# Kernel optimization log

Hardware: AMD Instinct MI355X
Metric: run time of the kernel (lower is better)

Reference implementation:

```python
import jax, jax.numpy as jnp
import numpy as np

NUM_CLASSES = 100
CLUSTERS_PER_CLASS = 64
LATENT_DIM = 128
BATCH = 32768


def setup_inputs() -> dict:
    key = jax.random.key(0)
    kx, kc, kl = jax.random.split(key, 3)
    x = jax.random.normal(kx, (BATCH, LATENT_DIM), dtype=jnp.float32)
    # nn.Parameter(torch.randn(C, Kc, D) * 0.1)
    centers = jax.random.normal(kc, (NUM_CLASSES, CLUSTERS_PER_CLASS, LATENT_DIM), dtype=jnp.float32) * 0.1
    labels = jax.random.randint(kl, (BATCH,), 0, NUM_CLASSES, dtype=jnp.int64)
    return {"x": x, "centers": centers, "labels": labels}


def reference(x, centers, labels):
    # [C, Kc, D] -> [K, D]
    all_centers = centers.reshape(-1, LATENT_DIM).astype(x.dtype)
    x2 = jnp.sum(x * x, axis=-1, keepdims=True)            # [B,1]
    c2 = jnp.sum(all_centers * all_centers, axis=-1)       # [K]
    sq = x2 + c2[None, :] - 2.0 * jnp.einsum('bd,kd->bk', x, all_centers)
    distances = jnp.sqrt(jnp.maximum(sq, 0.0))             # [B,K]
    closest_indices = jnp.argmin(distances, axis=1)        # [B]
    class_predictions = closest_indices // CLUSTERS_PER_CLASS
    cluster_assignments = closest_indices % CLUSTERS_PER_CLASS
    quantized_hard = all_centers[closest_indices]          # [B,D]
    min_distances = jnp.take_along_axis(distances, closest_indices[:, None], axis=1)[:, 0]
    # straight-through estimator (training path in the torch module)
    quantized = x + jax.lax.stop_gradient(quantized_hard - x)
    return quantized, cluster_assignments, min_distances, class_predictions
```

## Files before the change

kernel.cpp:

```cpp
#include <hip/hip_runtime.h>
#include <math.h>

#define BATCH  32768
#define D      128
#define K      6400
#define KC     64
#define ROWS_PER_BLOCK 128
#define CHUNK_C 128
#define HALVES 2
#define CHUNKS_PER_HALF 25

typedef _Float16 half8 __attribute__((ext_vector_type(8)));
typedef float    floatx4 __attribute__((ext_vector_type(4)));

typedef __attribute__((address_space(3))) unsigned       lds_uint;
typedef __attribute__((address_space(1))) const unsigned glb_uint;

__device__ __forceinline__ void async_lds16(const void* g, void* l) {
    __builtin_amdgcn_global_load_lds((glb_uint*)g, (lds_uint*)l, 16, 0, 0);
}

__global__ __launch_bounds__(256) void pack_kernel(const float* __restrict__ centers,
                                                   _Float16* __restrict__ wh,
                                                   float* __restrict__ c2n) {
    int tid = blockIdx.x * 256 + threadIdx.x;
    int ch = tid >> 11;
    int u  = (tid >> 7) & 15;
    int cw = tid & 127;
    int center = ch * CHUNK_C + cw;
    const float* src = centers + (size_t)center * D + u * 8;
    float4 a = *(const float4*)src;
    float4 b = *(const float4*)(src + 4);
    float f[8] = {a.x, a.y, a.z, a.w, b.x, b.y, b.z, b.w};
    half8 h;
#pragma unroll
    for (int j = 0; j < 8; ++j) h[j] = (_Float16)f[j];
    *(half8*)(wh + (size_t)tid * 8) = h;

    if (blockIdx.x < K / KC) {
        int c_local = threadIdx.x >> 2, part = threadIdx.x & 3;
        int c = blockIdx.x * 64 + c_local;
        const float4* p = (const float4*)(centers + (size_t)c * D + part * 32);
        float s = 0.f;
#pragma unroll
        for (int i = 0; i < 8; ++i) {
            float4 v = p[i];
            s = fmaf(v.x, v.x, s); s = fmaf(v.y, v.y, s);
            s = fmaf(v.z, v.z, s); s = fmaf(v.w, v.w, s);
        }
        s += __shfl_xor(s, 1, 64);
        s += __shfl_xor(s, 2, 64);
        if (part == 0) c2n[c] = -0.5f * s;
    }
}

__global__ __launch_bounds__(512, 4) void dist_kernel(
    const float* __restrict__ x, const float* __restrict__ centers,
    const _Float16* __restrict__ wh, const float* __restrict__ c2n,
    float* __restrict__ ws_sq, int* __restrict__ ws_ix) {
    __shared__ char lds[65536];

    const int t    = threadIdx.x;
    const int w    = t >> 6;
    const int L    = t & 63;
    const int quad = L >> 4;
    const int n16  = L & 15;
    const int rq      = w >> 1;
    const int chalf   = w & 1;
    const int half = blockIdx.y;
    const int gr0  = blockIdx.x * ROWS_PER_BLOCK;

    half8 Ah[2][4];
#pragma unroll
    for (int rt = 0; rt < 2; ++rt) {
        int r = gr0 + rq * 32 + rt * 16 + n16;
        const float* xr = x + (size_t)r * D + quad * 8;
#pragma unroll
        for (int ks = 0; ks < 4; ++ks) {
            float4 a = *(const float4*)(xr + ks * 32);
            float4 b = *(const float4*)(xr + ks * 32 + 4);
            float f[8] = {a.x, a.y, a.z, a.w, b.x, b.y, b.z, b.w};
            half8 h;
#pragma unroll
            for (int j = 0; j < 8; ++j) h[j] = (_Float16)f[j];
            Ah[rt][ks] = h;
        }
    }

    float b1[8], b2[8];
    int   j1_[8], j2_[8];
#pragma unroll
    for (int k = 0; k < 8; ++k) { b1[k] = -3.4e38f; b2[k] = -3.4e38f; j1_[k] = 0; j2_[k] = 0; }

    const char* gh = (const char*)wh + (size_t)half * CHUNKS_PER_HALF * 32768;

#pragma unroll
    for (int i = 0; i < 4; ++i) {
        int seg = w + i * 8;
        async_lds16(gh + seg * 1024 + L * 16, lds + seg * 1024);
    }
    __syncthreads();

    for (int ci = 0; ci < CHUNKS_PER_HALF; ++ci) {
        const char* cur = lds + (ci & 1) * 32768;
        if (ci + 1 < CHUNKS_PER_HALF) {
            const char* gn = gh + (ci + 1) * 32768;
            char* nxt = lds + ((ci + 1) & 1) * 32768;
#pragma unroll
            for (int i = 0; i < 4; ++i) {
                int seg = w + i * 8;
                async_lds16(gn + seg * 1024 + L * 16, nxt + seg * 1024);
            }
        }

        const int kbase = (half * CHUNKS_PER_HALF + ci) * CHUNK_C + chalf * 64;
        float c2v[4];
#pragma unroll
        for (int ct = 0; ct < 4; ++ct) c2v[ct] = c2n[kbase + ct * 16 + n16];

        floatx4 acc[2][4];
#pragma unroll
        for (int rt = 0; rt < 2; ++rt)
#pragma unroll
            for (int ct = 0; ct < 4; ++ct)
                acc[rt][ct] = (floatx4){c2v[ct], c2v[ct], c2v[ct], c2v[ct]};

#pragma unroll
        for (int ks = 0; ks < 4; ++ks) {
            const half8* pb = (const half8*)cur + (ks * 4 + quad) * 128 + chalf * 64 + n16;
#pragma unroll
            for (int ct = 0; ct < 4; ++ct) {
                half8 Bf = pb[ct * 16];
                acc[0][ct] = __builtin_amdgcn_mfma_f32_16x16x32_f16(Ah[0][ks], Bf, acc[0][ct], 0, 0, 0);
                acc[1][ct] = __builtin_amdgcn_mfma_f32_16x16x32_f16(Ah[1][ks], Bf, acc[1][ct], 0, 0, 0);
            }
        }

        int i0 = kbase + n16;
#pragma unroll
        for (int rt = 0; rt < 2; ++rt)
#pragma unroll
            for (int reg = 0; reg < 4; ++reg) {
                float s0 = acc[rt][0][reg], s1 = acc[rt][1][reg];
                float s2 = acc[rt][2][reg], s3 = acc[rt][3][reg];
                bool g01 = s1 > s0, g23 = s3 > s2;
                float m01 = g01 ? s1 : s0;  int x01 = g01 ? i0 + 16 : i0;
                float m23 = g23 ? s3 : s2;  int x23 = g23 ? i0 + 48 : i0 + 32;
                bool gq = m23 > m01;
                float v  = gq ? m23 : m01;  int vi = gq ? x23 : x01;
                int k = rt * 4 + reg;
                bool bet1 = v > b1[k];
                bool bet2 = v > b2[k];
                float nb2 = bet1 ? b1[k] : (bet2 ? v : b2[k]);
                int   nj2 = bet1 ? j1_[k] : (bet2 ? vi : j2_[k]);
                b1[k]  = bet1 ? v : b1[k];
                j1_[k] = bet1 ? vi : j1_[k];
                b2[k]  = nb2;
                j2_[k] = nj2;
            }

        __syncthreads();
    }

    int* candL = (int*)lds;

#pragma unroll
    for (int k = 0; k < 8; ++k) {
        float v1 = b1[k], v2 = b2[k];
        int   p1 = j1_[k], p2 = j2_[k];
#pragma unroll
        for (int m = 1; m < 8; m <<= 1) {
            float o1 = __shfl_xor(v1, m, 64), o2 = __shfl_xor(v2, m, 64);
            int   q1 = __shfl_xor(p1, m, 64), q2 = __shfl_xor(p2, m, 64);
            bool firstMine = (v1 > o1) || (v1 == o1 && p1 < q1);
            float nv1 = firstMine ? v1 : o1;  int np1 = firstMine ? p1 : q1;
            float cb  = firstMine ? o1 : v1;  int cpi = firstMine ? q1 : p1;
            float ob  = firstMine ? v2 : o2;  int obi = firstMine ? p2 : q2;
            bool secOwn = (ob > cb) || (ob == cb && obi < cpi);
            v1 = nv1; p1 = np1;
            v2 = secOwn ? ob : cb;  p2 = secOwn ? obi : cpi;
        }
        if ((n16 & 7) == 0) {
            int rloc = rq * 32 + (k >> 2) * 16 + quad * 4 + (k & 3);
            int g = chalf * 2 + (n16 >> 3);
            candL[rloc * 8 + g * 2 + 0] = p1;
            candL[rloc * 8 + g * 2 + 1] = p2;
        }
    }
    __syncthreads();

    {
        int r = t >> 2, p = t & 3;
        int ixa = candL[r * 8 + p * 2 + 0];
        int ixb = candL[r * 8 + p * 2 + 1];
        const float4* xr4 = (const float4*)(x + (size_t)(gr0 + r) * D);
        const float4* ca4 = (const float4*)(centers + (size_t)ixa * D);
        const float4* cb4 = (const float4*)(centers + (size_t)ixb * D);
        float dota = 0.f, dotb = 0.f, x2s = 0.f, c2a = 0.f, c2b = 0.f;
#pragma unroll
        for (int d4 = 0; d4 < 32; ++d4) {
            float4 xv = xr4[d4], av = ca4[d4], bv = cb4[d4];
            dota = fmaf(xv.x, av.x, dota); dota = fmaf(xv.y, av.y, dota);
            dota = fmaf(xv.z, av.z, dota); dota = fmaf(xv.w, av.w, dota);
            dotb = fmaf(xv.x, bv.x, dotb); dotb = fmaf(xv.y, bv.y, dotb);
            dotb = fmaf(xv.z, bv.z, dotb); dotb = fmaf(xv.w, bv.w, dotb);
            x2s = fmaf(xv.x, xv.x, x2s); x2s = fmaf(xv.y, xv.y, x2s);
            x2s = fmaf(xv.z, xv.z, x2s); x2s = fmaf(xv.w, xv.w, x2s);
            c2a = fmaf(av.x, av.x, c2a); c2a = fmaf(av.y, av.y, c2a);
            c2a = fmaf(av.z, av.z, c2a); c2a = fmaf(av.w, av.w, c2a);
            c2b = fmaf(bv.x, bv.x, c2b); c2b = fmaf(bv.y, bv.y, c2b);
            c2b = fmaf(bv.z, bv.z, c2b); c2b = fmaf(bv.w, bv.w, c2b);
        }
        float sqa = x2s + c2a - 2.f * dota;
        float sqb = x2s + c2b - 2.f * dotb;
        bool aw = (sqa < sqb) || (sqa == sqb && ixa < ixb);
        float sq = aw ? sqa : sqb;
        int   ix = aw ? ixa : ixb;
#pragma unroll
        for (int m = 1; m < 4; m <<= 1) {
            float osq = __shfl_xor(sq, m, 64);
            int   oix = __shfl_xor(ix, m, 64);
            if (osq < sq || (osq == sq && oix < ix)) { sq = osq; ix = oix; }
        }
        if (p == 0) {
            ws_sq[(size_t)half * BATCH + gr0 + r] = sq;
            ws_ix[(size_t)half * BATCH + gr0 + r] = ix;
        }
    }
}

__global__ __launch_bounds__(256) void final_kernel(
    const float* __restrict__ x, const float* __restrict__ centers,
    const float* __restrict__ ws_sq, const int* __restrict__ ws_ix,
    float* __restrict__ out) {
    int g = blockIdx.x * 256 + threadIdx.x;
    int row = g >> 5, d4 = g & 31;

    float sqa = ws_sq[row],         sqb = ws_sq[BATCH + row];
    int   ixa = ws_ix[row],         ixb = ws_ix[BATCH + row];
    bool aw = (sqa <= sqb);
    float sq = aw ? sqa : sqb;
    int   ix = aw ? ixa : ixb;

    float* out_clu = out + (size_t)BATCH * D;
    float* out_md  = out_clu + BATCH;
    float* out_cls = out_md + BATCH;
    if (d4 == 0) {
        out_md[row]  = sqrtf(fmaxf(sq, 0.f));
        out_clu[row] = (float)(ix & (KC - 1));
        out_cls[row] = (float)(ix >> 6);
    }

    float4 cv = ((const float4*)centers)[(size_t)ix * 32 + d4];
    float4 xv = ((const float4*)x)[(size_t)row * 32 + d4];
    float4 o;
    o.x = xv.x + (cv.x - xv.x);
    o.y = xv.y + (cv.y - xv.y);
    o.z = xv.z + (cv.z - xv.z);
    o.w = xv.w + (cv.w - xv.w);
    ((float4*)out)[(size_t)row * 32 + d4] = o;
}

extern "C" void kernel_launch(void* const* d_in, const int* in_sizes, int n_in,
                              void* d_out, int out_size, void* d_ws, size_t ws_size,
                              hipStream_t stream) {
    const float* x       = (const float*)d_in[0];
    const float* centers = (const float*)d_in[1];
    float* out = (float*)d_out;

    _Float16* wh    = (_Float16*)d_ws;
    float*    c2n   = (float*)(wh + (size_t)K * D);
    float*    ws_sq = c2n + K;
    int*      ws_ix = (int*)(ws_sq + HALVES * BATCH);

    pack_kernel<<<(K * 16) / 256, 256, 0, stream>>>(centers, wh, c2n);
    dim3 grid(BATCH / ROWS_PER_BLOCK, HALVES);
    dist_kernel<<<grid, 512, 0, stream>>>(x, centers, wh, c2n, ws_sq, ws_ix);
    final_kernel<<<(BATCH * 32) / 256, 256, 0, stream>>>(x, centers, ws_sq, ws_ix, out);
}
```

Measured before the change: 197.1 us.

## Pack distance and index into one key and split centers into quarters

```diff
diff --git a/kernel.cpp b/kernel.cpp
--- a/kernel.cpp
+++ b/kernel.cpp
@@ -5,10 +5,10 @@
 #define D      128
 #define K      6400
 #define KC     64
-#define ROWS_PER_BLOCK 128
-#define CHUNK_C 128
-#define HALVES 2
-#define CHUNKS_PER_HALF 25
+#define ROWS_PER_BLOCK 64
+#define GROUP_C 64
+#define QUARTERS 4
+#define GROUPS_PER_QUARTER 25
 
 typedef _Float16 half8 __attribute__((ext_vector_type(8)));
 typedef float    floatx4 __attribute__((ext_vector_type(4)));
@@ -22,12 +22,12 @@
 
 __global__ __launch_bounds__(256) void pack_kernel(const float* __restrict__ centers,
                                                    _Float16* __restrict__ wh,
-                                                   float* __restrict__ c2n) {
+                                                   float* __restrict__ c2h) {
     int tid = blockIdx.x * 256 + threadIdx.x;
-    int ch = tid >> 11;
-    int u  = (tid >> 7) & 15;
-    int cw = tid & 127;
-    int center = ch * CHUNK_C + cw;
+    int g  = tid >> 10;
+    int u  = (tid >> 6) & 15;
+    int cw = tid & 63;
+    int center = g * GROUP_C + cw;
     const float* src = centers + (size_t)center * D + u * 8;
     float4 a = *(const float4*)src;
     float4 b = *(const float4*)(src + 4);
@@ -50,15 +50,15 @@
         }
         s += __shfl_xor(s, 1, 64);
         s += __shfl_xor(s, 2, 64);
-        if (part == 0) c2n[c] = -0.5f * s;
-    }
-}
-
-__global__ __launch_bounds__(512, 4) void dist_kernel(
+        if (part == 0) c2h[c] = 0.5f * s;
+    }
+}
+
+__global__ __launch_bounds__(256, 5) void dist_kernel(
     const float* __restrict__ x, const float* __restrict__ centers,
-    const _Float16* __restrict__ wh, const float* __restrict__ c2n,
+    const _Float16* __restrict__ wh, const float* __restrict__ c2h,
     float* __restrict__ ws_sq, int* __restrict__ ws_ix) {
-    __shared__ char lds[65536];
+    __shared__ char lds[32768];
 
     const int t    = threadIdx.x;
     const int w    = t >> 6;
@@ -67,14 +67,16 @@
     const int n16  = L & 15;
     const int rq      = w >> 1;
     const int chalf   = w & 1;
-    const int half = blockIdx.y;
+    const int q    = blockIdx.y;
     const int gr0  = blockIdx.x * ROWS_PER_BLOCK;
 
     half8 Ah[2][4];
+    float x2f[2];
 #pragma unroll
     for (int rt = 0; rt < 2; ++rt) {
         int r = gr0 + rq * 32 + rt * 16 + n16;
         const float* xr = x + (size_t)r * D + quad * 8;
+        float s = 0.f;
 #pragma unroll
         for (int ks = 0; ks < 4; ++ks) {
             float4 a = *(const float4*)(xr + ks * 32);
@@ -82,82 +84,86 @@
             float f[8] = {a.x, a.y, a.z, a.w, b.x, b.y, b.z, b.w};
             half8 h;
 #pragma unroll
-            for (int j = 0; j < 8; ++j) h[j] = (_Float16)f[j];
+            for (int j = 0; j < 8; ++j) {
+                s = fmaf(f[j], f[j], s);
+                h[j] = (_Float16)(-f[j]);
+            }
             Ah[rt][ks] = h;
         }
-    }
-
-    float b1[8], b2[8];
-    int   j1_[8], j2_[8];
-#pragma unroll
-    for (int k = 0; k < 8; ++k) { b1[k] = -3.4e38f; b2[k] = -3.4e38f; j1_[k] = 0; j2_[k] = 0; }
-
-    const char* gh = (const char*)wh + (size_t)half * CHUNKS_PER_HALF * 32768;
+        s += __shfl_xor(s, 16, 64);
+        s += __shfl_xor(s, 32, 64);
+        x2f[rt] = s;
+    }
+    float x2q[2][4];
+#pragma unroll
+    for (int rt = 0; rt < 2; ++rt)
+#pragma unroll
+        for (int reg = 0; reg < 4; ++reg)
+            x2q[rt][reg] = 0.5f * __shfl(x2f[rt], quad * 4 + reg, 64);
+
+    unsigned b1[8], b2[8];
+#pragma unroll
+    for (int k = 0; k < 8; ++k) { b1[k] = 0xFFFFFFFFu; b2[k] = 0xFFFFFFFFu; }
+
+    const char* gh = (const char*)wh + (size_t)q * GROUPS_PER_QUARTER * 16384;
 
 #pragma unroll
     for (int i = 0; i < 4; ++i) {
-        int seg = w + i * 8;
+        int seg = w + i * 4;
         async_lds16(gh + seg * 1024 + L * 16, lds + seg * 1024);
     }
     __syncthreads();
 
-    for (int ci = 0; ci < CHUNKS_PER_HALF; ++ci) {
-        const char* cur = lds + (ci & 1) * 32768;
-        if (ci + 1 < CHUNKS_PER_HALF) {
-            const char* gn = gh + (ci + 1) * 32768;
-            char* nxt = lds + ((ci + 1) & 1) * 32768;
+    for (int ci = 0; ci < GROUPS_PER_QUARTER; ++ci) {
+        const char* cur = lds + (ci & 1) * 16384;
+        if (ci + 1 < GROUPS_PER_QUARTER) {
+            const char* gn = gh + (ci + 1) * 16384;
+            char* nxt = lds + ((ci + 1) & 1) * 16384;
 #pragma unroll
             for (int i = 0; i < 4; ++i) {
-                int seg = w + i * 8;
+                int seg = w + i * 4;
                 async_lds16(gn + seg * 1024 + L * 16, nxt + seg * 1024);
             }
         }
 
-        const int kbase = (half * CHUNKS_PER_HALF + ci) * CHUNK_C + chalf * 64;
-        float c2v[4];
-#pragma unroll
-        for (int ct = 0; ct < 4; ++ct) c2v[ct] = c2n[kbase + ct * 16 + n16];
-
-        floatx4 acc[2][4];
+        const int kbase = (q * GROUPS_PER_QUARTER + ci) * GROUP_C + chalf * 32;
+        float c2v[2];
+        c2v[0] = c2h[kbase + n16];
+        c2v[1] = c2h[kbase + 16 + n16];
+
+        floatx4 acc[2][2];
 #pragma unroll
         for (int rt = 0; rt < 2; ++rt)
 #pragma unroll
-            for (int ct = 0; ct < 4; ++ct)
-                acc[rt][ct] = (floatx4){c2v[ct], c2v[ct], c2v[ct], c2v[ct]};
+            for (int ct = 0; ct < 2; ++ct)
+#pragma unroll
+                for (int reg = 0; reg < 4; ++reg)
+                    acc[rt][ct][reg] = c2v[ct] + x2q[rt][reg];
 
 #pragma unroll
         for (int ks = 0; ks < 4; ++ks) {
-            const half8* pb = (const half8*)cur + (ks * 4 + quad) * 128 + chalf * 64 + n16;
-#pragma unroll
-            for (int ct = 0; ct < 4; ++ct) {
-                half8 Bf = pb[ct * 16];
-                acc[0][ct] = __builtin_amdgcn_mfma_f32_16x16x32_f16(Ah[0][ks], Bf, acc[0][ct], 0, 0, 0);
-                acc[1][ct] = __builtin_amdgcn_mfma_f32_16x16x32_f16(Ah[1][ks], Bf, acc[1][ct], 0, 0, 0);
+            const half8* pb = (const half8*)cur + (ks * 4 + quad) * 64 + chalf * 32 + n16;
+            half8 B0 = pb[0];
+            half8 B1 = pb[16];
+            acc[0][0] = __builtin_amdgcn_mfma_f32_16x16x32_f16(Ah[0][ks], B0, acc[0][0], 0, 0, 0);
+            acc[1][0] = __builtin_amdgcn_mfma_f32_16x16x32_f16(Ah[1][ks], B0, acc[1][0], 0, 0, 0);
+            acc[0][1] = __builtin_amdgcn_mfma_f32_16x16x32_f16(Ah[0][ks], B1, acc[0][1], 0, 0, 0);
+            acc[1][1] = __builtin_amdgcn_mfma_f32_16x16x32_f16(Ah[1][ks], B1, acc[1][1], 0, 0, 0);
+        }
+
+        unsigned lc0 = (unsigned)(ci * 2);
+        unsigned lc1 = (unsigned)(ci * 2 + 1);
+#pragma unroll
+        for (int rt = 0; rt < 2; ++rt)
+#pragma unroll
+            for (int reg = 0; reg < 4; ++reg) {
+                unsigned k0 = (__float_as_uint(acc[rt][0][reg]) & 0xFFFFFFC0u) | lc0;
+                unsigned k1 = (__float_as_uint(acc[rt][1][reg]) & 0xFFFFFFC0u) | lc1;
+                unsigned kq = min(k0, k1);
+                int k = rt * 4 + reg;
+                b2[k] = min(b2[k], max(b1[k], kq));
+                b1[k] = min(b1[k], kq);
             }
-        }
-
-        int i0 = kbase + n16;
-#pragma unroll
-        for (int rt = 0; rt < 2; ++rt)
-#pragma unroll
-            for (int reg = 0; reg < 4; ++reg) {
-                float s0 = acc[rt][0][reg], s1 = acc[rt][1][reg];
-                float s2 = acc[rt][2][reg], s3 = acc[rt][3][reg];
-                bool g01 = s1 > s0, g23 = s3 > s2;
-                float m01 = g01 ? s1 : s0;  int x01 = g01 ? i0 + 16 : i0;
-                float m23 = g23 ? s3 : s2;  int x23 = g23 ? i0 + 48 : i0 + 32;
-                bool gq = m23 > m01;
-                float v  = gq ? m23 : m01;  int vi = gq ? x23 : x01;
-                int k = rt * 4 + reg;
-                bool bet1 = v > b1[k];
-                bool bet2 = v > b2[k];
-                float nb2 = bet1 ? b1[k] : (bet2 ? v : b2[k]);
-                int   nj2 = bet1 ? j1_[k] : (bet2 ? vi : j2_[k]);
-                b1[k]  = bet1 ? v : b1[k];
-                j1_[k] = bet1 ? vi : j1_[k];
-                b2[k]  = nb2;
-                j2_[k] = nj2;
-            }
 
         __syncthreads();
     }
@@ -166,17 +172,21 @@
 
 #pragma unroll
     for (int k = 0; k < 8; ++k) {
-        float v1 = b1[k], v2 = b2[k];
-        int   p1 = j1_[k], p2 = j2_[k];
+        unsigned v1 = b1[k], v2 = b2[k];
+        int lc1i = (int)(v1 & 63u), lc2i = (int)(v2 & 63u);
+        int p1 = (q * GROUPS_PER_QUARTER + (lc1i >> 1)) * GROUP_C + chalf * 32 + (lc1i & 1) * 16 + n16;
+        int p2 = (q * GROUPS_PER_QUARTER + (lc2i >> 1)) * GROUP_C + chalf * 32 + (lc2i & 1) * 16 + n16;
 #pragma unroll
         for (int m = 1; m < 8; m <<= 1) {
-            float o1 = __shfl_xor(v1, m, 64), o2 = __shfl_xor(v2, m, 64);
-            int   q1 = __shfl_xor(p1, m, 64), q2 = __shfl_xor(p2, m, 64);
-            bool firstMine = (v1 > o1) || (v1 == o1 && p1 < q1);
-            float nv1 = firstMine ? v1 : o1;  int np1 = firstMine ? p1 : q1;
-            float cb  = firstMine ? o1 : v1;  int cpi = firstMine ? q1 : p1;
-            float ob  = firstMine ? v2 : o2;  int obi = firstMine ? p2 : q2;
-            bool secOwn = (ob > cb) || (ob == cb && obi < cpi);
+            unsigned o1 = (unsigned)__shfl_xor((int)v1, m, 64);
+            unsigned o2 = (unsigned)__shfl_xor((int)v2, m, 64);
+            int      q1 = __shfl_xor(p1, m, 64);
+            int      q2 = __shfl_xor(p2, m, 64);
+            bool firstMine = (v1 < o1) || (v1 == o1 && p1 < q1);
+            unsigned nv1 = firstMine ? v1 : o1;  int np1 = firstMine ? p1 : q1;
+            unsigned cb  = firstMine ? o1 : v1;  int cpi = firstMine ? q1 : p1;
+            unsigned ob  = firstMine ? v2 : o2;  int obi = firstMine ? p2 : q2;
+            bool secOwn = (ob < cb) || (ob == cb && obi < cpi);
             v1 = nv1; p1 = np1;
             v2 = secOwn ? ob : cb;  p2 = secOwn ? obi : cpi;
         }
@@ -223,8 +233,8 @@
             if (osq < sq || (osq == sq && oix < ix)) { sq = osq; ix = oix; }
         }
         if (p == 0) {
-            ws_sq[(size_t)half * BATCH + gr0 + r] = sq;
-            ws_ix[(size_t)half * BATCH + gr0 + r] = ix;
+            ws_sq[(size_t)q * BATCH + gr0 + r] = sq;
+            ws_ix[(size_t)q * BATCH + gr0 + r] = ix;
         }
     }
 }
@@ -236,11 +246,14 @@
     int g = blockIdx.x * 256 + threadIdx.x;
     int row = g >> 5, d4 = g & 31;
 
-    float sqa = ws_sq[row],         sqb = ws_sq[BATCH + row];
-    int   ixa = ws_ix[row],         ixb = ws_ix[BATCH + row];
-    bool aw = (sqa <= sqb);
-    float sq = aw ? sqa : sqb;
-    int   ix = aw ? ixa : ixb;
+    float sq = ws_sq[row];
+    int   ix = ws_ix[row];
+#pragma unroll
+    for (int h = 1; h < QUARTERS; ++h) {
+        float s2 = ws_sq[(size_t)h * BATCH + row];
+        int   i2 = ws_ix[(size_t)h * BATCH + row];
+        if (s2 < sq) { sq = s2; ix = i2; }
+    }
 
     float* out_clu = out + (size_t)BATCH * D;
     float* out_md  = out_clu + BATCH;
@@ -269,12 +282,12 @@
     float* out = (float*)d_out;
 
     _Float16* wh    = (_Float16*)d_ws;
-    float*    c2n   = (float*)(wh + (size_t)K * D);
-    float*    ws_sq = c2n + K;
-    int*      ws_ix = (int*)(ws_sq + HALVES * BATCH);
-
-    pack_kernel<<<(K * 16) / 256, 256, 0, stream>>>(centers, wh, c2n);
-    dim3 grid(BATCH / ROWS_PER_BLOCK, HALVES);
-    dist_kernel<<<grid, 512, 0, stream>>>(x, centers, wh, c2n, ws_sq, ws_ix);
+    float*    c2h   = (float*)(wh + (size_t)K * D);
+    float*    ws_sq = c2h + K;
+    int*      ws_ix = (int*)(ws_sq + QUARTERS * BATCH);
+
+    pack_kernel<<<(K * 16) / 256, 256, 0, stream>>>(centers, wh, c2h);
+    dim3 grid(BATCH / ROWS_PER_BLOCK, QUARTERS);
+    dist_kernel<<<grid, 256, 0, stream>>>(x, centers, wh, c2h, ws_sq, ws_ix);
     final_kernel<<<(BATCH * 32) / 256, 256, 0, stream>>>(x, centers, ws_sq, ws_ix, out);
 }
```

Result: slower. 243.1 us (+23.3%).
